# Optimization experiments

Measured on AMD Instinct MI355X. Metric: run time of the kernel, lower is better.

The kernel has to match this reference:

```python
import jax, jax.numpy as jnp
import numpy as np

T, B, I, H, O = 512, 64, 512, 1024, 512


def setup_inputs() -> dict:
    key = jax.random.key(0)
    ks = jax.random.split(key, 5)
    s_gate = 1.0 / np.sqrt(I + H)  # torch Linear default init scale
    s_out = 1.0 / np.sqrt(H)
    return {
        "x": jax.random.normal(ks[0], (T, B, I), dtype=jnp.float32),
        "Wz": jax.random.normal(ks[1], (I + H, H), dtype=jnp.float32) * s_gate,
        "bz": jnp.zeros((H,), dtype=jnp.float32),
        "Wr": jax.random.normal(ks[2], (I + H, H), dtype=jnp.float32) * s_gate,
        "br": jnp.zeros((H,), dtype=jnp.float32),
        "Wh": jax.random.normal(ks[3], (I + H, H), dtype=jnp.float32) * s_gate,
        "bh": jnp.zeros((H,), dtype=jnp.float32),
        "Wo": jax.random.normal(ks[4], (H, O), dtype=jnp.float32) * s_out,
        "bo": jnp.zeros((O,), dtype=jnp.float32),
    }


def reference(x, Wz, bz, Wr, br, Wh, bh, Wo, bo):
    # Hand-rolled GRU cell (note: candidate uses sigmoid, as in the source),
    # scanned over time; dropout omitted (predict / eval path).
    batch = x.shape[1]
    h0 = jnp.zeros((batch, Wz.shape[1]), dtype=x.dtype)

    def step(h, x_t):
        xc = jnp.concatenate([x_t, h], axis=1)               # [B, I+H]
        z = jax.nn.sigmoid(xc @ Wz + bz)                     # [B, H]
        r = jax.nn.sigmoid(xc @ Wr + br)                     # [B, H]
        xh = jnp.concatenate([x_t, h * r], axis=1)           # [B, I+H]
        h_new = z * h + (1.0 - z) * jax.nn.sigmoid(xh @ Wh + bh)
        out = h_new @ Wo + bo                                # [B, O]
        return h_new, out

    _, outputs = jax.lax.scan(step, h0, x)                   # [T, B, O]
    return outputs
```

## Files before the change

kernel.cpp:

```cpp
#include <hip/hip_runtime.h>
#include <math.h>

#define TT 512
#define BB 64
#define II 512
#define HH 1024
#define OO 512
#define KK 1536

#define GRID 256
#define NTHR 512

__device__ __forceinline__ float sigmoidf_(float v) {
    return 1.0f / (1.0f + __expf(-v));
}

__device__ __forceinline__ void st_sys(float* p, float v) {
    asm volatile("global_store_dword %0, %1, off sc0 sc1"
                 :: "v"(p), "v"(v) : "memory");
}

#define DOT4(accv, av, wv) do { \
    (accv) = fmaf((av).x, (wv).x, (accv)); \
    (accv) = fmaf((av).y, (wv).y, (accv)); \
    (accv) = fmaf((av).z, (wv).z, (accv)); \
    (accv) = fmaf((av).w, (wv).w, (accv)); } while (0)

__device__ __forceinline__ void gbar(unsigned* cb, unsigned target8, int tid, int grp)
{
    asm volatile("s_waitcnt vmcnt(0)" ::: "memory");
    __syncthreads();
    if (tid == 0) {
        unsigned old = __hip_atomic_fetch_add(&cb[grp * 32], 1u,
                           __ATOMIC_RELAXED, __HIP_MEMORY_SCOPE_AGENT);
        if ((old & 31u) == 31u)
            __hip_atomic_fetch_add(&cb[256], 1u,
                __ATOMIC_RELAXED, __HIP_MEMORY_SCOPE_AGENT);
        while (__hip_atomic_load(&cb[256], __ATOMIC_RELAXED,
                   __HIP_MEMORY_SCOPE_AGENT) < target8)
            __builtin_amdgcn_s_sleep(1);
    }
    __syncthreads();
    __builtin_amdgcn_fence(__ATOMIC_ACQUIRE, "agent");
}

__global__ void zero_ctr(unsigned* c) {
    for (int i = 0; i < 8; ++i) c[i * 32] = 0u;
    c[256] = 0u;
}

__global__ __launch_bounds__(NTHR, 2) void gru_fused(
    const float* __restrict__ x,
    const float* __restrict__ Wz, const float* __restrict__ bz,
    const float* __restrict__ Wr, const float* __restrict__ br,
    const float* __restrict__ Wh, const float* __restrict__ bh,
    const float* __restrict__ Wo, const float* __restrict__ bo,
    float* __restrict__ out, float* __restrict__ ws)
{
    __shared__ float wgA[8 * KK];
    __shared__ float whB[4 * KK];
    __shared__ float woO[2 * HH];

    float* h  = ws;
    float* hr = ws + 1 * 65536;
    float* zb = ws + 2 * 65536;
    unsigned* cb = (unsigned*)(ws + 3 * 65536);

    const int bid = blockIdx.x;
    const int tid = threadIdx.x;
    const int grp = bid >> 5;

    const bool is_r = (bid & 128) != 0;
    const float* Wg = is_r ? Wr : Wz;
    const int j0  = (bid & 127) * 8;
    const int j0h = bid * 4;
    const int j0o = bid * 2;

    for (int i = tid; i < KK * 8; i += NTHR)
        wgA[(i & 7) * KK + (i >> 3)] = Wg[(size_t)(i >> 3) * HH + j0 + (i & 7)];
    for (int i = tid; i < KK * 4; i += NTHR)
        whB[(i & 3) * KK + (i >> 2)] = Wh[(size_t)(i >> 2) * HH + j0h + (i & 3)];
    for (int i = tid; i < HH * 2; i += NTHR)
        woO[(i & 1) * HH + (i >> 1)] = Wo[(size_t)(i >> 1) * OO + j0o + (i & 1)];

    {
        int g = bid * NTHR + tid;
        if (g < BB * HH) st_sys(&h[g], 0.0f);
    }

    const int ko = tid & 31;
    const int bg = tid >> 5;
    const int b0 = bg * 4;

    const int ciA = ko >> 3, cjA = ko & 7;
    const int bA = b0 + ciA, jA = j0 + cjA;
    const float biasA = is_r ? br[jA] : bz[jA];

    const int ciB = ko >> 2, cjB = ko & 3;
    const int bB = b0 + ciB, jB = j0h + cjB;
    const float biasB = bh[jB];

    const int ciO = ko >> 1, cjO = ko & 1;
    const int bO = b0 + ciO, jO = j0o + cjO;
    const float biasO = bo[jO];

    const float4* wg4 = (const float4*)wgA;
    const float4* wh4 = (const float4*)whB;
    const float4* wo4 = (const float4*)woO;

    unsigned tgt = 8;
    gbar(cb, tgt, tid, grp);

    for (int t = 0; t < TT; ++t) {
        const float* xt = x + (size_t)t * BB * II;

        const float4* xp0 = (const float4*)(xt + (size_t)(b0 + 0) * II);
        const float4* xp1 = (const float4*)(xt + (size_t)(b0 + 1) * II);
        const float4* xp2 = (const float4*)(xt + (size_t)(b0 + 2) * II);
        const float4* xp3 = (const float4*)(xt + (size_t)(b0 + 3) * II);
        const float4* hp0 = (const float4*)(h + (size_t)(b0 + 0) * HH);
        const float4* hp1 = (const float4*)(h + (size_t)(b0 + 1) * HH);
        const float4* hp2 = (const float4*)(h + (size_t)(b0 + 2) * HH);
        const float4* hp3 = (const float4*)(h + (size_t)(b0 + 3) * HH);

        {
            const size_t iA = (size_t)bA * HH + jA;
            float hpre = 0.f;
            if (is_r) hpre = h[iA];

            float acc[4][8];
            #pragma unroll
            for (int i = 0; i < 4; ++i)
                #pragma unroll
                for (int j = 0; j < 8; ++j) acc[i][j] = 0.f;

            #pragma unroll
            for (int u = 0; u < 12; ++u) {
                const int kq = ko + 32 * u;
                float4 av[4];
                if (u < 4) {
                    av[0] = xp0[kq]; av[1] = xp1[kq];
                    av[2] = xp2[kq]; av[3] = xp3[kq];
                } else {
                    av[0] = hp0[kq - 128]; av[1] = hp1[kq - 128];
                    av[2] = hp2[kq - 128]; av[3] = hp3[kq - 128];
                }
                #pragma unroll
                for (int jh = 0; jh < 2; ++jh) {
                    float4 wv[4];
                    #pragma unroll
                    for (int jj = 0; jj < 4; ++jj)
                        wv[jj] = wg4[(jh * 4 + jj) * 384 + kq];
                    #pragma unroll
                    for (int i = 0; i < 4; ++i)
                        #pragma unroll
                        for (int jj = 0; jj < 4; ++jj)
                            DOT4(acc[i][jh * 4 + jj], av[i], wv[jj]);
                }
            }
            float cellA = 0.f;
            #pragma unroll
            for (int i = 0; i < 4; ++i)
                #pragma unroll
                for (int j = 0; j < 8; ++j) {
                    float v = acc[i][j];
                    v += __shfl_xor(v, 1);
                    v += __shfl_xor(v, 2);
                    v += __shfl_xor(v, 4);
                    v += __shfl_xor(v, 8);
                    v += __shfl_xor(v, 16);
                    if (ciA == i && cjA == j) cellA = v;
                }
            float val = sigmoidf_(biasA + cellA);
            if (is_r) st_sys(&hr[iA], hpre * val);
            else      st_sys(&zb[iA], val);
        }

        {
            float acc[4][2];
            #pragma unroll
            for (int i = 0; i < 4; ++i) { acc[i][0] = 0.f; acc[i][1] = 0.f; }

            #pragma unroll
            for (int u = 0; u < 8; ++u) {
                const int kq = ko + 32 * u;
                float4 av[4];
                av[0] = hp0[kq]; av[1] = hp1[kq];
                av[2] = hp2[kq]; av[3] = hp3[kq];
                float4 w0 = wo4[kq];
                float4 w1 = wo4[256 + kq];
                #pragma unroll
                for (int i = 0; i < 4; ++i) {
                    DOT4(acc[i][0], av[i], w0);
                    DOT4(acc[i][1], av[i], w1);
                }
            }
            float cellO = 0.f;
            #pragma unroll
            for (int i = 0; i < 4; ++i)
                #pragma unroll
                for (int j = 0; j < 2; ++j) {
                    float v = acc[i][j];
                    v += __shfl_xor(v, 1);
                    v += __shfl_xor(v, 2);
                    v += __shfl_xor(v, 4);
                    v += __shfl_xor(v, 8);
                    v += __shfl_xor(v, 16);
                    if (ciO == i && cjO == j) cellO = v;
                }
            if (ko < 8 && t > 0)
                out[(size_t)(t - 1) * BB * OO + (size_t)bO * OO + jO]
                    = biasO + cellO;
        }

        tgt += 8; gbar(cb, tgt, tid, grp);

        {
            const size_t iB = (size_t)bB * HH + jB;
            float zpre = 0.f, hpre2 = 0.f;
            if (ko < 16) { zpre = zb[iB]; hpre2 = h[iB]; }

            const float4* rp0 = (const float4*)(hr + (size_t)(b0 + 0) * HH);
            const float4* rp1 = (const float4*)(hr + (size_t)(b0 + 1) * HH);
            const float4* rp2 = (const float4*)(hr + (size_t)(b0 + 2) * HH);
            const float4* rp3 = (const float4*)(hr + (size_t)(b0 + 3) * HH);

            float acc[4][4];
            #pragma unroll
            for (int i = 0; i < 4; ++i)
                #pragma unroll
                for (int j = 0; j < 4; ++j) acc[i][j] = 0.f;

            #pragma unroll
            for (int u = 0; u < 12; ++u) {
                const int kq = ko + 32 * u;
                float4 av[4];
                if (u < 4) {
                    av[0] = xp0[kq]; av[1] = xp1[kq];
                    av[2] = xp2[kq]; av[3] = xp3[kq];
                } else {
                    av[0] = rp0[kq - 128]; av[1] = rp1[kq - 128];
                    av[2] = rp2[kq - 128]; av[3] = rp3[kq - 128];
                }
                float4 wv[4];
                #pragma unroll
                for (int jj = 0; jj < 4; ++jj)
                    wv[jj] = wh4[jj * 384 + kq];
                #pragma unroll
                for (int i = 0; i < 4; ++i)
                    #pragma unroll
                    for (int jj = 0; jj < 4; ++jj)
                        DOT4(acc[i][jj], av[i], wv[jj]);
            }
            float cellB = 0.f;
            #pragma unroll
            for (int i = 0; i < 4; ++i)
                #pragma unroll
                for (int j = 0; j < 4; ++j) {
                    float v = acc[i][j];
                    v += __shfl_xor(v, 1);
                    v += __shfl_xor(v, 2);
                    v += __shfl_xor(v, 4);
                    v += __shfl_xor(v, 8);
                    v += __shfl_xor(v, 16);
                    if (ciB == i && cjB == j) cellB = v;
                }
            if (ko < 16) {
                float cv = sigmoidf_(biasB + cellB);
                st_sys(&h[iB], zpre * hpre2 + (1.0f - zpre) * cv);
            }
        }
        tgt += 8; gbar(cb, tgt, tid, grp);
    }

    {
        const float4* hp0 = (const float4*)(h + (size_t)(b0 + 0) * HH);
        const float4* hp1 = (const float4*)(h + (size_t)(b0 + 1) * HH);
        const float4* hp2 = (const float4*)(h + (size_t)(b0 + 2) * HH);
        const float4* hp3 = (const float4*)(h + (size_t)(b0 + 3) * HH);
        float acc[4][2];
        #pragma unroll
        for (int i = 0; i < 4; ++i) { acc[i][0] = 0.f; acc[i][1] = 0.f; }
        #pragma unroll
        for (int u = 0; u < 8; ++u) {
            const int kq = ko + 32 * u;
            float4 av[4];
            av[0] = hp0[kq]; av[1] = hp1[kq];
            av[2] = hp2[kq]; av[3] = hp3[kq];
            float4 w0 = wo4[kq];
            float4 w1 = wo4[256 + kq];
            #pragma unroll
            for (int i = 0; i < 4; ++i) {
                DOT4(acc[i][0], av[i], w0);
                DOT4(acc[i][1], av[i], w1);
            }
        }
        float cellO = 0.f;
        #pragma unroll
        for (int i = 0; i < 4; ++i)
            #pragma unroll
            for (int j = 0; j < 2; ++j) {
                float v = acc[i][j];
                v += __shfl_xor(v, 1);
                v += __shfl_xor(v, 2);
                v += __shfl_xor(v, 4);
                v += __shfl_xor(v, 8);
                v += __shfl_xor(v, 16);
                if (ciO == i && cjO == j) cellO = v;
            }
        if (ko < 8)
            out[(size_t)(TT - 1) * BB * OO + (size_t)bO * OO + jO]
                = biasO + cellO;
    }
}

extern "C" void kernel_launch(void* const* d_in, const int* in_sizes, int n_in,
                              void* d_out, int out_size, void* d_ws, size_t ws_size,
                              hipStream_t stream)
{
    (void)in_sizes; (void)n_in; (void)out_size; (void)ws_size;
    const float* x  = (const float*)d_in[0];
    const float* Wz = (const float*)d_in[1];
    const float* bz = (const float*)d_in[2];
    const float* Wr = (const float*)d_in[3];
    const float* br = (const float*)d_in[4];
    const float* Wh = (const float*)d_in[5];
    const float* bh = (const float*)d_in[6];
    const float* Wo = (const float*)d_in[7];
    const float* bo = (const float*)d_in[8];
    float* out = (float*)d_out;
    float* ws  = (float*)d_ws;

    zero_ctr<<<1, 1, 0, stream>>>((unsigned*)(ws + 3 * 65536));

    void* args[] = { (void*)&x, (void*)&Wz, (void*)&bz, (void*)&Wr, (void*)&br,
                     (void*)&Wh, (void*)&bh, (void*)&Wo, (void*)&bo,
                     (void*)&out, (void*)&ws };
    hipLaunchCooperativeKernel(reinterpret_cast<void*>(gru_fused),
                               dim3(GRID), dim3(NTHR), args, 0, stream);
}
```

Measured before the change: 29.05 ms.

## Use reduce-scatter shuffles, fuse output projection into gate pass, cache x in registers

Replaces the per-accumulator full butterfly allreduce (5 shuffles for each of 32/16/8 values) with a recursive-halving reduce-scatter, so each lane ends up with its own cell using about N-1 shuffles in total. Fuses the Wo output projection into the gate GEMM loop, so the h loads are shared instead of re-read. Keeps the x_t tiles in registers for reuse in the candidate pass. The cost is higher register pressure (32+8 accumulators plus 16 cached float4s) under launch_bounds(512,2), which could cause spills.

```diff
diff --git a/kernel.cpp b/kernel.cpp
--- a/kernel.cpp
+++ b/kernel.cpp
@@ -49,6 +49,111 @@
     c[256] = 0u;
 }
 
+__device__ __forceinline__ float rs32(float (&v)[32], int ko)
+{
+    const bool h16 = (ko & 16) != 0;
+    float a[16];
+    #pragma unroll
+    for (int k = 0; k < 16; ++k) {
+        float send = h16 ? v[k] : v[k + 16];
+        float keep = h16 ? v[k + 16] : v[k];
+        a[k] = keep + __shfl_xor(send, 16);
+    }
+    const bool h8 = (ko & 8) != 0;
+    float b[8];
+    #pragma unroll
+    for (int k = 0; k < 8; ++k) {
+        float send = h8 ? a[k] : a[k + 8];
+        float keep = h8 ? a[k + 8] : a[k];
+        b[k] = keep + __shfl_xor(send, 8);
+    }
+    const bool h4 = (ko & 4) != 0;
+    float c[4];
+    #pragma unroll
+    for (int k = 0; k < 4; ++k) {
+        float send = h4 ? b[k] : b[k + 4];
+        float keep = h4 ? b[k + 4] : b[k];
+        c[k] = keep + __shfl_xor(send, 4);
+    }
+    const bool h2 = (ko & 2) != 0;
+    float d[2];
+    #pragma unroll
+    for (int k = 0; k < 2; ++k) {
+        float send = h2 ? c[k] : c[k + 2];
+        float keep = h2 ? c[k + 2] : c[k];
+        d[k] = keep + __shfl_xor(send, 2);
+    }
+    const bool h1 = (ko & 1) != 0;
+    float send = h1 ? d[0] : d[1];
+    float keep = h1 ? d[1] : d[0];
+    return keep + __shfl_xor(send, 1);
+}
+
+__device__ __forceinline__ float rs16(float (&v)[16], int ko)
+{
+    float a[16];
+    #pragma unroll
+    for (int k = 0; k < 16; ++k) a[k] = v[k] + __shfl_xor(v[k], 16);
+    const bool h8 = (ko & 8) != 0;
+    float b[8];
+    #pragma unroll
+    for (int k = 0; k < 8; ++k) {
+        float send = h8 ? a[k] : a[k + 8];
+        float keep = h8 ? a[k + 8] : a[k];
+        b[k] = keep + __shfl_xor(send, 8);
+    }
+    const bool h4 = (ko & 4) != 0;
+    float c[4];
+    #pragma unroll
+    for (int k = 0; k < 4; ++k) {
+        float send = h4 ? b[k] : b[k + 4];
+        float keep = h4 ? b[k + 4] : b[k];
+        c[k] = keep + __shfl_xor(send, 4);
+    }
+    const bool h2 = (ko & 2) != 0;
+    float d[2];
+    #pragma unroll
+    for (int k = 0; k < 2; ++k) {
+        float send = h2 ? c[k] : c[k + 2];
+        float keep = h2 ? c[k + 2] : c[k];
+        d[k] = keep + __shfl_xor(send, 2);
+    }
+    const bool h1 = (ko & 1) != 0;
+    float send = h1 ? d[0] : d[1];
+    float keep = h1 ? d[1] : d[0];
+    return keep + __shfl_xor(send, 1);
+}
+
+__device__ __forceinline__ float rs8(float (&v)[8], int ko)
+{
+    float a[8];
+    #pragma unroll
+    for (int k = 0; k < 8; ++k) {
+        float t = v[k] + __shfl_xor(v[k], 16);
+        a[k] = t + __shfl_xor(t, 8);
+    }
+    const bool h4 = (ko & 4) != 0;
+    float c[4];
+    #pragma unroll
+    for (int k = 0; k < 4; ++k) {
+        float send = h4 ? a[k] : a[k + 4];
+        float keep = h4 ? a[k + 4] : a[k];
+        c[k] = keep + __shfl_xor(send, 4);
+    }
+    const bool h2 = (ko & 2) != 0;
+    float d[2];
+    #pragma unroll
+    for (int k = 0; k < 2; ++k) {
+        float send = h2 ? c[k] : c[k + 2];
+        float keep = h2 ? c[k + 2] : c[k];
+        d[k] = keep + __shfl_xor(send, 2);
+    }
+    const bool h1 = (ko & 1) != 0;
+    float send = h1 ? d[0] : d[1];
+    float keep = h1 ? d[1] : d[0];
+    return keep + __shfl_xor(send, 1);
+}
+
 __global__ __launch_bounds__(NTHR, 2) void gru_fused(
     const float* __restrict__ x,
     const float* __restrict__ Wz, const float* __restrict__ bz,
@@ -92,16 +197,13 @@
     const int bg = tid >> 5;
     const int b0 = bg * 4;
 
-    const int ciA = ko >> 3, cjA = ko & 7;
-    const int bA = b0 + ciA, jA = j0 + cjA;
+    const int bA = b0 + (ko >> 3), jA = j0 + (ko & 7);
     const float biasA = is_r ? br[jA] : bz[jA];
 
-    const int ciB = ko >> 2, cjB = ko & 3;
-    const int bB = b0 + ciB, jB = j0h + cjB;
+    const int bB = b0 + (ko >> 2), jB = j0h + (ko & 3);
     const float biasB = bh[jB];
 
-    const int ciO = ko >> 1, cjO = ko & 1;
-    const int bO = b0 + ciO, jO = j0o + cjO;
+    const int bO = b0 + (ko >> 1), jO = j0o + (ko & 1);
     const float biasO = bo[jO];
 
     const float4* wg4 = (const float4*)wgA;
@@ -123,148 +225,99 @@
         const float4* hp2 = (const float4*)(h + (size_t)(b0 + 2) * HH);
         const float4* hp3 = (const float4*)(h + (size_t)(b0 + 3) * HH);
 
+        float4 xr[4][4];
+
+        const size_t iA = (size_t)bA * HH + jA;
+        const size_t iB = (size_t)bB * HH + jB;
         {
-            const size_t iA = (size_t)bA * HH + jA;
             float hpre = 0.f;
             if (is_r) hpre = h[iA];
-
-            float acc[4][8];
-            #pragma unroll
-            for (int i = 0; i < 4; ++i)
-                #pragma unroll
-                for (int j = 0; j < 8; ++j) acc[i][j] = 0.f;
+            float hpre2 = 0.f;
+            if (ko < 16) hpre2 = h[iB];
+
+            float accA[32], accO[8];
+            #pragma unroll
+            for (int c = 0; c < 32; ++c) accA[c] = 0.f;
+            #pragma unroll
+            for (int c = 0; c < 8; ++c) accO[c] = 0.f;
 
             #pragma unroll
             for (int u = 0; u < 12; ++u) {
                 const int kq = ko + 32 * u;
-                float4 av[4];
+                float4 av0, av1, av2, av3;
                 if (u < 4) {
-                    av[0] = xp0[kq]; av[1] = xp1[kq];
-                    av[2] = xp2[kq]; av[3] = xp3[kq];
+                    av0 = xp0[kq]; av1 = xp1[kq];
+                    av2 = xp2[kq]; av3 = xp3[kq];
+                    xr[u][0] = av0; xr[u][1] = av1;
+                    xr[u][2] = av2; xr[u][3] = av3;
                 } else {
-                    av[0] = hp0[kq - 128]; av[1] = hp1[kq - 128];
-                    av[2] = hp2[kq - 128]; av[3] = hp3[kq - 128];
+                    av0 = hp0[kq - 128]; av1 = hp1[kq - 128];
+                    av2 = hp2[kq - 128]; av3 = hp3[kq - 128];
                 }
                 #pragma unroll
-                for (int jh = 0; jh < 2; ++jh) {
-                    float4 wv[4];
-                    #pragma unroll
-                    for (int jj = 0; jj < 4; ++jj)
-                        wv[jj] = wg4[(jh * 4 + jj) * 384 + kq];
-                    #pragma unroll
-                    for (int i = 0; i < 4; ++i)
-                        #pragma unroll
-                        for (int jj = 0; jj < 4; ++jj)
-                            DOT4(acc[i][jh * 4 + jj], av[i], wv[jj]);
+                for (int jj = 0; jj < 8; ++jj) {
+                    float4 wv = wg4[jj * 384 + kq];
+                    DOT4(accA[0 * 8 + jj], av0, wv);
+                    DOT4(accA[1 * 8 + jj], av1, wv);
+                    DOT4(accA[2 * 8 + jj], av2, wv);
+                    DOT4(accA[3 * 8 + jj], av3, wv);
+                }
+                if (u >= 4) {
+                    float4 w0 = wo4[kq - 128];
+                    float4 w1 = wo4[256 + (kq - 128)];
+                    DOT4(accO[0], av0, w0); DOT4(accO[1], av0, w1);
+                    DOT4(accO[2], av1, w0); DOT4(accO[3], av1, w1);
+                    DOT4(accO[4], av2, w0); DOT4(accO[5], av2, w1);
+                    DOT4(accO[6], av3, w0); DOT4(accO[7], av3, w1);
                 }
             }
-            float cellA = 0.f;
-            #pragma unroll
-            for (int i = 0; i < 4; ++i)
-                #pragma unroll
-                for (int j = 0; j < 8; ++j) {
-                    float v = acc[i][j];
-                    v += __shfl_xor(v, 1);
-                    v += __shfl_xor(v, 2);
-                    v += __shfl_xor(v, 4);
-                    v += __shfl_xor(v, 8);
-                    v += __shfl_xor(v, 16);
-                    if (ciA == i && cjA == j) cellA = v;
-                }
+
+            float cellA = rs32(accA, ko);
             float val = sigmoidf_(biasA + cellA);
             if (is_r) st_sys(&hr[iA], hpre * val);
             else      st_sys(&zb[iA], val);
-        }
-
-        {
-            float acc[4][2];
-            #pragma unroll
-            for (int i = 0; i < 4; ++i) { acc[i][0] = 0.f; acc[i][1] = 0.f; }
-
-            #pragma unroll
-            for (int u = 0; u < 8; ++u) {
-                const int kq = ko + 32 * u;
-                float4 av[4];
-                av[0] = hp0[kq]; av[1] = hp1[kq];
-                av[2] = hp2[kq]; av[3] = hp3[kq];
-                float4 w0 = wo4[kq];
-                float4 w1 = wo4[256 + kq];
-                #pragma unroll
-                for (int i = 0; i < 4; ++i) {
-                    DOT4(acc[i][0], av[i], w0);
-                    DOT4(acc[i][1], av[i], w1);
-                }
-            }
-            float cellO = 0.f;
-            #pragma unroll
-            for (int i = 0; i < 4; ++i)
-                #pragma unroll
-                for (int j = 0; j < 2; ++j) {
-                    float v = acc[i][j];
-                    v += __shfl_xor(v, 1);
-                    v += __shfl_xor(v, 2);
-                    v += __shfl_xor(v, 4);
-                    v += __shfl_xor(v, 8);
-                    v += __shfl_xor(v, 16);
-                    if (ciO == i && cjO == j) cellO = v;
-                }
+
+            float cellO = rs8(accO, ko);
             if (ko < 8 && t > 0)
                 out[(size_t)(t - 1) * BB * OO + (size_t)bO * OO + jO]
                     = biasO + cellO;
-        }
-
-        tgt += 8; gbar(cb, tgt, tid, grp);
-
-        {
-            const size_t iB = (size_t)bB * HH + jB;
-            float zpre = 0.f, hpre2 = 0.f;
-            if (ko < 16) { zpre = zb[iB]; hpre2 = h[iB]; }
+
+            tgt += 8; gbar(cb, tgt, tid, grp);
+
+            float zpre = 0.f;
+            if (ko < 16) zpre = zb[iB];
 
             const float4* rp0 = (const float4*)(hr + (size_t)(b0 + 0) * HH);
             const float4* rp1 = (const float4*)(hr + (size_t)(b0 + 1) * HH);
             const float4* rp2 = (const float4*)(hr + (size_t)(b0 + 2) * HH);
             const float4* rp3 = (const float4*)(hr + (size_t)(b0 + 3) * HH);
 
-            float acc[4][4];
-            #pragma unroll
-            for (int i = 0; i < 4; ++i)
-                #pragma unroll
-                for (int j = 0; j < 4; ++j) acc[i][j] = 0.f;
+            float accB[16];
+            #pragma unroll
+            for (int c = 0; c < 16; ++c) accB[c] = 0.f;
 
             #pragma unroll
             for (int u = 0; u < 12; ++u) {
                 const int kq = ko + 32 * u;
-                float4 av[4];
+                float4 av0, av1, av2, av3;
                 if (u < 4) {
-                    av[0] = xp0[kq]; av[1] = xp1[kq];
-                    av[2] = xp2[kq]; av[3] = xp3[kq];
+                    av0 = xr[u][0]; av1 = xr[u][1];
+                    av2 = xr[u][2]; av3 = xr[u][3];
                 } else {
-                    av[0] = rp0[kq - 128]; av[1] = rp1[kq - 128];
-                    av[2] = rp2[kq - 128]; av[3] = rp3[kq - 128];
-                }
-                float4 wv[4];
+                    av0 = rp0[kq - 128]; av1 = rp1[kq - 128];
+                    av2 = rp2[kq - 128]; av3 = rp3[kq - 128];
+                }
                 #pragma unroll
-                for (int jj = 0; jj < 4; ++jj)
-                    wv[jj] = wh4[jj * 384 + kq];
-                #pragma unroll
-                for (int i = 0; i < 4; ++i)
-                    #pragma unroll
-                    for (int jj = 0; jj < 4; ++jj)
-                        DOT4(acc[i][jj], av[i], wv[jj]);
+                for (int jj = 0; jj < 4; ++jj) {
+                    float4 wv = wh4[jj * 384 + kq];
+                    DOT4(accB[0 * 4 + jj], av0, wv);
+                    DOT4(accB[1 * 4 + jj], av1, wv);
+                    DOT4(accB[2 * 4 + jj], av2, wv);
+                    DOT4(accB[3 * 4 + jj], av3, wv);
+                }
             }
-            float cellB = 0.f;
-            #pragma unroll
-            for (int i = 0; i < 4; ++i)
-                #pragma unroll
-                for (int j = 0; j < 4; ++j) {
-                    float v = acc[i][j];
-                    v += __shfl_xor(v, 1);
-                    v += __shfl_xor(v, 2);
-                    v += __shfl_xor(v, 4);
-                    v += __shfl_xor(v, 8);
-                    v += __shfl_xor(v, 16);
-                    if (ciB == i && cjB == j) cellB = v;
-                }
+
+            float cellB = rs16(accB, ko);
             if (ko < 16) {
                 float cv = sigmoidf_(biasB + cellB);
                 st_sys(&h[iB], zpre * hpre2 + (1.0f - zpre) * cv);
@@ -278,36 +331,22 @@
         const float4* hp1 = (const float4*)(h + (size_t)(b0 + 1) * HH);
         const float4* hp2 = (const float4*)(h + (size_t)(b0 + 2) * HH);
         const float4* hp3 = (const float4*)(h + (size_t)(b0 + 3) * HH);
-        float acc[4][2];
+        float accO[8];
         #pragma unroll
-        for (int i = 0; i < 4; ++i) { acc[i][0] = 0.f; acc[i][1] = 0.f; }
+        for (int c = 0; c < 8; ++c) accO[c] = 0.f;
         #pragma unroll
         for (int u = 0; u < 8; ++u) {
             const int kq = ko + 32 * u;
-            float4 av[4];
-            av[0] = hp0[kq]; av[1] = hp1[kq];
-            av[2] = hp2[kq]; av[3] = hp3[kq];
+            float4 av0 = hp0[kq], av1 = hp1[kq];
+            float4 av2 = hp2[kq], av3 = hp3[kq];
             float4 w0 = wo4[kq];
             float4 w1 = wo4[256 + kq];
-            #pragma unroll
-            for (int i = 0; i < 4; ++i) {
-                DOT4(acc[i][0], av[i], w0);
-                DOT4(acc[i][1], av[i], w1);
-            }
+            DOT4(accO[0], av0, w0); DOT4(accO[1], av0, w1);
+            DOT4(accO[2], av1, w0); DOT4(accO[3], av1, w1);
+            DOT4(accO[4], av2, w0); DOT4(accO[5], av2, w1);
+            DOT4(accO[6], av3, w0); DOT4(accO[7], av3, w1);
         }
-        float cellO = 0.f;
-        #pragma unroll
-        for (int i = 0; i < 4; ++i)
-            #pragma unroll
-            for (int j = 0; j < 2; ++j) {
-                float v = acc[i][j];
-                v += __shfl_xor(v, 1);
-                v += __shfl_xor(v, 2);
-                v += __shfl_xor(v, 4);
-                v += __shfl_xor(v, 8);
-                v += __shfl_xor(v, 16);
-                if (ciO == i && cjO == j) cellO = v;
-            }
+        float cellO = rs8(accO, ko);
         if (ko < 8)
             out[(size_t)(TT - 1) * BB * OO + (size_t)bO * OO + jO]
                 = biasO + cellO;
```

New measurement: 29.46 ms. About the same (+1.4%).
